# Performance work log

Hardware: AMD Instinct MI355X
Metric: run time of the kernel (lower is better)

Reference implementation:

```python
import jax, jax.numpy as jnp
import numpy as np

B, NP, KP = 1024, 196, 4  # batch, patches per image (14x14), pixels per patch
THR_HI, THR_LO, W_LO = 0.8, 0.5, 0.5


def setup_inputs() -> dict:
    key = jax.random.key(0)
    k1, k2, k3, k4 = jax.random.split(key, 4)
    x = jax.random.normal(k1, (B, 1, 28, 28), dtype=jnp.float32)
    phi = jax.random.uniform(k2, (B, NP, KP), dtype=jnp.float32) * (2.0 * np.pi)
    W_lin = jax.random.normal(k3, (10, NP * KP), dtype=jnp.float32) * 0.05
    b_lin = jax.random.normal(k4, (10,), dtype=jnp.float32) * 0.05
    return {"x": x, "phi": phi, "W_lin": W_lin, "b_lin": b_lin}


def _extract_patches(x):
    # x: [B,1,28,28] -> non-overlapping 2x2 patches, flatten order (kh, kw)
    b = x.shape[0]
    p = x[:, 0].reshape(b, 14, 2, 14, 2)            # (b, hp, kh, wp, kw)
    p = jnp.transpose(p, (0, 1, 3, 2, 4))           # (b, hp, wp, kh, kw)
    return p.reshape(b, NP, KP)


def _forward(x, phi, W_lin, b_lin):
    theta = _extract_patches(x)                     # [B,196,4] RY angles
    # Analytic 4-qubit circuit: z_i = <Z_i before CNOTs> = cos(theta)cos(phi);
    # CNOT chain maps Z_k -> Z_0...Z_k, so expvals are the cumulative product.
    z = jnp.cos(theta) * jnp.cos(phi)               # [B,196,4]
    expvals = jnp.cumprod(z, axis=-1)               # [B,196,4]

    # Graph is built on detached states in the original (patch_out.detach())
    states = jax.lax.stop_gradient(expvals)
    nrm = states / (jnp.linalg.norm(states, axis=-1, keepdims=True) + 1e-12)
    fid = jnp.einsum("bnd,bmd->bnm", nrm, nrm) ** 2  # squared cosine fidelity
    w = jnp.where(fid >= THR_HI, 1.0, jnp.where(fid >= THR_LO, W_LO, 0.0))
    w = w * (1.0 - jnp.eye(NP, dtype=w.dtype))       # no self-edges (i<j pairs)
    deg = jnp.sum(w, axis=-1)                        # [B,196]
    # smooth = I + L, L = D - W
    smooth = jnp.eye(NP, dtype=w.dtype)[None] + (jnp.zeros_like(w) + jnp.eye(NP)[None] * deg[:, :, None] - w)
    smoothed = jnp.einsum("bnm,bmd->bnd", smooth, expvals)  # [B,196,4]

    feats = smoothed.reshape(smoothed.shape[0], -1)  # [B,784]
    logits = feats @ W_lin.T + b_lin
    return jax.nn.log_softmax(logits, axis=-1)


def reference(x, phi, W_lin, b_lin):
    return _forward(x, phi, W_lin, b_lin)
```

## Files before the change

### kernel.cpp

```cpp
#include <hip/hip_runtime.h>
#include <math.h>

#define NP 196
#define NCLS 10

__global__ __launch_bounds__(256) void quanv_fused_kernel(
    const float* __restrict__ x,
    const float* __restrict__ phi,
    const float* __restrict__ W,
    const float* __restrict__ bl,
    float* __restrict__ out)
{
    const int b    = blockIdx.x;
    const int t    = threadIdx.x;
    const int wave = t >> 6;
    const int lane = t & 63;

    __shared__ float4 e_s[NP];
    __shared__ float  inv_s[NP];
    __shared__ float2 thr_s[NP];
    __shared__ float4 pa_s[4 * NP];
    __shared__ float  pd_s[4 * NP];
    __shared__ float4 feat_s[NP];
    __shared__ float  logit_s[NCLS];

    const float* xb = x + (size_t)b * 784;
    const float* pb = phi + (size_t)b * 784;

    if (t < NP) {
        const int hp = t / 14, wp = t - hp * 14;
        const int r0 = hp * 2, c0 = wp * 2;
        float th0 = xb[r0 * 28 + c0];
        float th1 = xb[r0 * 28 + c0 + 1];
        float th2 = xb[(r0 + 1) * 28 + c0];
        float th3 = xb[(r0 + 1) * 28 + c0 + 1];
        float4 ph = *(const float4*)(pb + t * 4);
        float z0 = __cosf(th0) * __cosf(ph.x);
        float z1 = __cosf(th1) * __cosf(ph.y);
        float z2 = __cosf(th2) * __cosf(ph.z);
        float z3 = __cosf(th3) * __cosf(ph.w);
        float e0 = z0;
        float e1 = e0 * z1;
        float e2 = e1 * z2;
        float e3 = e2 * z3;
        e_s[t] = make_float4(e0, e1, e2, e3);
        float nn = sqrtf(e0 * e0 + e1 * e1 + e2 * e2 + e3 * e3) + 1e-12f;
        inv_s[t] = 1.0f / nn;
        thr_s[t] = make_float2(0.8944271909999159f * nn,
                               0.7071067811865476f * nn);
    }
    __syncthreads();

    if (lane < 49) {
        float4 qn[4];
        float4 a[4];
        float  deg[4];
        #pragma unroll
        for (int k = 0; k < 4; ++k) {
            const int n = lane + 49 * k;
            float4 q = e_s[n];
            float iv = inv_s[n];
            qn[k] = make_float4(q.x * iv, q.y * iv, q.z * iv, q.w * iv);
            a[k] = make_float4(0.f, 0.f, 0.f, 0.f);
            deg[k] = 0.f;
        }
        const int m0 = wave * 49;
        #pragma unroll 7
        for (int m = m0; m < m0 + 49; ++m) {
            float4 em = e_s[m];
            float2 th = thr_s[m];
            #pragma unroll
            for (int k = 0; k < 4; ++k) {
                float d  = qn[k].x * em.x + qn[k].y * em.y + qn[k].z * em.z + qn[k].w * em.w;
                float ad = fabsf(d);
                float w  = (ad >= th.x) ? 1.0f : ((ad >= th.y) ? 0.5f : 0.0f);
                deg[k] += w;
                a[k].x += w * em.x;
                a[k].y += w * em.y;
                a[k].z += w * em.z;
                a[k].w += w * em.w;
            }
        }
        #pragma unroll
        for (int k = 0; k < 4; ++k) {
            pa_s[wave * NP + lane + 49 * k] = a[k];
            pd_s[wave * NP + lane + 49 * k] = deg[k];
        }
    }
    __syncthreads();

    if (t < NP) {
        float4 e  = e_s[t];
        float  iv = inv_s[t];
        float2 th = thr_s[t];
        float4 at = make_float4(0.f, 0.f, 0.f, 0.f);
        float  dt = 0.f;
        #pragma unroll
        for (int w = 0; w < 4; ++w) {
            float4 p = pa_s[w * NP + t];
            at.x += p.x; at.y += p.y; at.z += p.z; at.w += p.w;
            dt += pd_s[w * NP + t];
        }
        float4 qnn = make_float4(e.x * iv, e.y * iv, e.z * iv, e.w * iv);
        float d   = qnn.x * e.x + qnn.y * e.y + qnn.z * e.z + qnn.w * e.w;
        float ad  = fabsf(d);
        float w   = (ad >= th.x) ? 1.0f : ((ad >= th.y) ? 0.5f : 0.0f);
        dt -= w;
        at.x -= w * e.x; at.y -= w * e.y; at.z -= w * e.z; at.w -= w * e.w;
        const float s = 1.0f + dt;
        feat_s[t] = make_float4(s * e.x - at.x, s * e.y - at.y,
                                s * e.z - at.z, s * e.w - at.w);
    }
    __syncthreads();

    if (t < NCLS * 16) {
        const int j  = t >> 4;
        const int sl = t & 15;
        const float4* wr = (const float4*)(W + j * 784);
        float p = 0.f;
        for (int i = sl; i < NP; i += 16) {
            float4 f  = feat_s[i];
            float4 w4 = wr[i];
            p += f.x * w4.x + f.y * w4.y + f.z * w4.z + f.w * w4.w;
        }
        #pragma unroll
        for (int off = 8; off > 0; off >>= 1)
            p += __shfl_down(p, off, 16);
        if (sl == 0) logit_s[j] = p + bl[j];
    }
    __syncthreads();

    if (t < NCLS) {
        float mx = -INFINITY;
        #pragma unroll
        for (int j = 0; j < NCLS; ++j) mx = fmaxf(mx, logit_s[j]);
        float sum = 0.f;
        #pragma unroll
        for (int j = 0; j < NCLS; ++j) sum += expf(logit_s[j] - mx);
        out[(size_t)b * NCLS + t] = logit_s[t] - mx - logf(sum);
    }
}

extern "C" void kernel_launch(void* const* d_in, const int* in_sizes, int n_in,
                              void* d_out, int out_size, void* d_ws, size_t ws_size,
                              hipStream_t stream) {
    const float* x   = (const float*)d_in[0];
    const float* phi = (const float*)d_in[1];
    const float* W   = (const float*)d_in[2];
    const float* bl  = (const float*)d_in[3];
    float* out = (float*)d_out;

    const int B = in_sizes[0] / 784;
    quanv_fused_kernel<<<dim3(B), dim3(256), 0, stream>>>(x, phi, W, bl, out);
}
```

Measured before the change: 23.72 us.

## Use all 64 lanes for pairwise graph pass, split 4 tail patches across lanes

Originally only 49 of 64 lanes per wave worked on the pairwise fidelity/adjacency loop, with each lane handling 4 rows. Now every lane handles 3 rows (lane+64k), covering 192 patches, and the remaining 4 patches are spread over the whole wave: 16 slices per patch, reduced with xor shuffles. Launch bounds also request 4 blocks per SM/CU to encourage lower register use. This shortens the serial inner loop per lane, at the cost of an extra shuffle-reduction step and possible register pressure.

New measurement: 22.48 us. -5.2%, faster.

```diff
diff --git a/kernel.cpp b/kernel.cpp
--- a/kernel.cpp
+++ b/kernel.cpp
@@ -4,7 +4,7 @@
 #define NP 196
 #define NCLS 10
 
-__global__ __launch_bounds__(256) void quanv_fused_kernel(
+__global__ __launch_bounds__(256, 4) void quanv_fused_kernel(
     const float* __restrict__ x,
     const float* __restrict__ phi,
     const float* __restrict__ W,
@@ -51,40 +51,72 @@
     }
     __syncthreads();
 
-    if (lane < 49) {
-        float4 qn[4];
-        float4 a[4];
-        float  deg[4];
+    float4 qn[3];
+    float4 a[3];
+    float  deg[3];
+    #pragma unroll
+    for (int k = 0; k < 3; ++k) {
+        const int n = lane + 64 * k;
+        float4 q = e_s[n];
+        float iv = inv_s[n];
+        qn[k] = make_float4(q.x * iv, q.y * iv, q.z * iv, q.w * iv);
+        a[k] = make_float4(0.f, 0.f, 0.f, 0.f);
+        deg[k] = 0.f;
+    }
+    const int m0 = wave * 49;
+    #pragma unroll 7
+    for (int m = m0; m < m0 + 49; ++m) {
+        float4 em = e_s[m];
+        float2 th = thr_s[m];
         #pragma unroll
-        for (int k = 0; k < 4; ++k) {
-            const int n = lane + 49 * k;
-            float4 q = e_s[n];
-            float iv = inv_s[n];
-            qn[k] = make_float4(q.x * iv, q.y * iv, q.z * iv, q.w * iv);
-            a[k] = make_float4(0.f, 0.f, 0.f, 0.f);
-            deg[k] = 0.f;
+        for (int k = 0; k < 3; ++k) {
+            float d  = qn[k].x * em.x + qn[k].y * em.y + qn[k].z * em.z + qn[k].w * em.w;
+            float ad = fabsf(d);
+            float w  = (ad >= th.x) ? 1.0f : ((ad >= th.y) ? 0.5f : 0.0f);
+            deg[k] += w;
+            a[k].x += w * em.x;
+            a[k].y += w * em.y;
+            a[k].z += w * em.z;
+            a[k].w += w * em.w;
         }
-        const int m0 = wave * 49;
-        #pragma unroll 7
-        for (int m = m0; m < m0 + 49; ++m) {
+    }
+    #pragma unroll
+    for (int k = 0; k < 3; ++k) {
+        pa_s[wave * NP + lane + 64 * k] = a[k];
+        pd_s[wave * NP + lane + 64 * k] = deg[k];
+    }
+
+    {
+        const int nt    = 192 + (lane & 3);
+        const int slice = lane >> 2;
+        float4 q = e_s[nt];
+        float iv = inv_s[nt];
+        float4 qt = make_float4(q.x * iv, q.y * iv, q.z * iv, q.w * iv);
+        float4 at = make_float4(0.f, 0.f, 0.f, 0.f);
+        float  dt = 0.f;
+        for (int m = m0 + slice; m < m0 + 49; m += 16) {
             float4 em = e_s[m];
             float2 th = thr_s[m];
-            #pragma unroll
-            for (int k = 0; k < 4; ++k) {
-                float d  = qn[k].x * em.x + qn[k].y * em.y + qn[k].z * em.z + qn[k].w * em.w;
-                float ad = fabsf(d);
-                float w  = (ad >= th.x) ? 1.0f : ((ad >= th.y) ? 0.5f : 0.0f);
-                deg[k] += w;
-                a[k].x += w * em.x;
-                a[k].y += w * em.y;
-                a[k].z += w * em.z;
-                a[k].w += w * em.w;
-            }
+            float d  = qt.x * em.x + qt.y * em.y + qt.z * em.z + qt.w * em.w;
+            float ad = fabsf(d);
+            float w  = (ad >= th.x) ? 1.0f : ((ad >= th.y) ? 0.5f : 0.0f);
+            dt += w;
+            at.x += w * em.x;
+            at.y += w * em.y;
+            at.z += w * em.z;
+            at.w += w * em.w;
         }
         #pragma unroll
-        for (int k = 0; k < 4; ++k) {
-            pa_s[wave * NP + lane + 49 * k] = a[k];
-            pd_s[wave * NP + lane + 49 * k] = deg[k];
+        for (int off = 4; off <= 32; off <<= 1) {
+            at.x += __shfl_xor(at.x, off, 64);
+            at.y += __shfl_xor(at.y, off, 64);
+            at.z += __shfl_xor(at.z, off, 64);
+            at.w += __shfl_xor(at.w, off, 64);
+            dt   += __shfl_xor(dt,   off, 64);
+        }
+        if (lane < 4) {
+            pa_s[wave * NP + 192 + lane] = at;
+            pd_s[wave * NP + 192 + lane] = dt;
         }
     }
     __syncthreads();
@@ -101,10 +133,10 @@
             at.x += p.x; at.y += p.y; at.z += p.z; at.w += p.w;
             dt += pd_s[w * NP + t];
         }
-        float4 qnn = make_float4(e.x * iv, e.y * iv, e.z * iv, e.w * iv);
-        float d   = qnn.x * e.x + qnn.y * e.y + qnn.z * e.z + qnn.w * e.w;
-        float ad  = fabsf(d);
-        float w   = (ad >= th.x) ? 1.0f : ((ad >= th.y) ? 0.5f : 0.0f);
+        float qx = e.x * iv, qy = e.y * iv, qz = e.z * iv, qw = e.w * iv;
+        float d  = qx * e.x + qy * e.y + qz * e.z + qw * e.w;
+        float ad = fabsf(d);
+        float w  = (ad >= th.x) ? 1.0f : ((ad >= th.y) ? 0.5f : 0.0f);
         dt -= w;
         at.x -= w * e.x; at.y -= w * e.y; at.z -= w * e.z; at.w -= w * e.w;
         const float s = 1.0f + dt;
```
